# Optimization experiments

Measured on AMD Instinct MI355X. Metric: run time of the kernel, lower is better.

Reference implementation:

```python
import jax, jax.numpy as jnp
import numpy as np

SIGMA = 300.0      # args.sigma (temporal gaussian kernel width, frames)
DECAY = 0.9        # args.memory_decay; avg() uses weight = 1/decay per older entry
W_TIME = 1.0       # args.temporal_weight
ORIG_LOSS = 1.0    # args.originalloss_weight
EPS = 1e-7         # BCE clamp


def _get_msg(bank_values, bank_times, bank_mask, ids, times, future):
    """Vectorized MessagePassing.get_msg: per-(id,time) gather of stored
    messages, temporal-kernel + decay weighted average. Mirrors avg():
    out = sum_i dw_i * kernel_i * v_i / sum_i dw_i, dw_i = (1/decay)^rank_i
    with rank over entries passing the past/future condition, zeros if empty."""
    vals = bank_values[ids]                      # [N, M, C]
    ts = bank_times[ids].astype(jnp.float32)     # [N, M]
    mk = bank_mask[ids]                          # [N, M]
    t0 = times.astype(jnp.float32)[:, None]      # [N, 1]
    cond = (ts > t0) if future else (ts < t0)
    m = (mk & cond).astype(vals.dtype)           # [N, M]
    kern = jnp.exp(-((ts - t0) ** 2) / (2.0 * SIGMA ** 2))
    rank = jnp.cumsum(m, axis=1) - m             # exclusive rank among valid entries
    dw = ((1.0 / DECAY) ** rank) * m             # decay weights, masked
    num = jnp.einsum('nm,nmc->nc', dw * kern, vals)
    den = jnp.sum(dw, axis=1, keepdims=True)     # denominator excludes kernel (as avg())
    msg = jnp.where(den > 0, num / jnp.maximum(den, EPS), 0.0)
    return msg * W_TIME


def _bce(p, t):
    p = jnp.clip(p, EPS, 1.0 - EPS)
    return -jnp.mean(t * jnp.log(p) + (1.0 - t) * jnp.log(1.0 - p))


def setup_inputs() -> dict:
    key = jax.random.key(0)
    k = jax.random.split(key, 8)
    N, C, NUM_IDS, M = 512, 157, 10000, 20
    return {
        'a': jax.random.normal(k[0], (N, C), jnp.float32),
        'aa': jax.random.normal(k[1], (N, C, C), jnp.float32),
        'target': jax.random.uniform(k[2], (N, C), jnp.float32),
        'bank_values': jax.random.uniform(k[3], (NUM_IDS, M, C), jnp.float32),
        'bank_times': jax.random.randint(k[4], (NUM_IDS, M), 0, 1000, jnp.int32),
        'bank_mask': jnp.ones((NUM_IDS, M), dtype=bool),
        'ids': jax.random.randint(k[5], (N,), 0, NUM_IDS, jnp.int32),
        'times': jax.random.randint(k[6], (N,), 0, 1000, jnp.int32),
    }


def reference(a, aa, target, bank_values, bank_times, bank_mask, ids, times):
    # msg/fmsg come from stored (detached) data in the original
    msg = jax.lax.stop_gradient(_get_msg(bank_values, bank_times, bank_mask, ids, times, future=False))
    fmsg = jax.lax.stop_gradient(_get_msg(bank_values, bank_times, bank_mask, ids, times, future=True))
    # qa = a + sum_i aa[n,i,j]*msg[n,i] + sum_j aa[n,i,j]*fmsg[n,j]
    qa = a + jnp.einsum('nij,ni->nj', aa, msg) + jnp.einsum('nij,nj->ni', aa, fmsg)
    qa = jax.nn.sigmoid(qa)
    loss = _bce(qa, target) + _bce(jax.nn.sigmoid(a), target) * ORIG_LOSS
    # training, adjustment=False: pastloss = futureloss = 0
    loss = loss / 3.0
    return qa, loss
```

## Files before the change

kernel.cpp:

```cpp
#include <hip/hip_runtime.h>
#include <math.h>

#define N 512
#define C 157
#define M 20
#define NW 8

__device__ __forceinline__ float sigmoidf_(float x) {
    return 1.0f / (1.0f + __expf(-x));
}

__global__ __launch_bounds__(512) void atf_main_kernel(
    const float* __restrict__ a,
    const float* __restrict__ aa,
    const float* __restrict__ target,
    const float* __restrict__ bank_values,
    const int* __restrict__ bank_times,
    const int* __restrict__ bank_mask,
    const int* __restrict__ ids,
    const int* __restrict__ times,
    float* __restrict__ out,
    float* __restrict__ loss_part)
{
    const int n    = blockIdx.x;
    const int tid  = threadIdx.x;
    const int wave = tid >> 6;
    const int lane = tid & 63;

    __shared__ float s_ts[M];
    __shared__ int   s_mk[M];
    __shared__ float s_msg[C];
    __shared__ float s_fmsg[C];
    __shared__ float s_rowp[8][C];
    __shared__ float s_colp[NW][C];
    __shared__ float s_red[NW];

    const int   id = ids[n];
    const float t0 = (float)times[n];

    const float* aan = aa + (size_t)n * C * C;
    const int j0 = lane, j1 = lane + 64, j2 = lane + 128;
    const bool ok1 = (j1 < C), ok2 = (j2 < C);

    float a0, a1, a2, b0, b1, b2;
    {
        const float* rA = aan + wave * C;
        a0 = rA[j0]; a1 = ok1 ? rA[j1] : 0.0f; a2 = ok2 ? rA[j2] : 0.0f;
        const float* rB = aan + (wave + NW) * C;
        b0 = rB[j0]; b1 = ok1 ? rB[j1] : 0.0f; b2 = ok2 ? rB[j2] : 0.0f;
    }
    float av = 0.0f, tv = 0.0f;
    if (tid < C) {
        av = a[(size_t)n * C + tid];
        tv = target[(size_t)n * C + tid];
    }

    if (tid < M) {
        s_ts[tid] = (float)bank_times[(size_t)id * M + tid];
        s_mk[tid] = (bank_mask[(size_t)id * M + tid] != 0) ? 1 : 0;
    }
    __syncthreads();

    if (tid < C) {
        const float inv2s2 = 1.0f / (2.0f * 300.0f * 300.0f);
        const float INVDEC = 1.0f / 0.9f;
        float accP = 0.f, accF = 0.f, denP = 0.f, denF = 0.f;
        float wP = 1.f, wF = 1.f;
        const float* vb = bank_values + (size_t)id * M * C + tid;
        #pragma unroll
        for (int m = 0; m < M; ++m) {
            const float ts = s_ts[m];
            const float d  = ts - t0;
            const float kern = __expf(-d * d * inv2s2);
            const float v = vb[m * C];
            const bool mk = (s_mk[m] != 0);
            if (mk && ts < t0) { accP += wP * kern * v; denP += wP; wP *= INVDEC; }
            if (mk && ts > t0) { accF += wF * kern * v; denF += wF; wF *= INVDEC; }
        }
        s_msg[tid]  = (denP > 0.f) ? accP / fmaxf(denP, 1e-7f) : 0.0f;
        s_fmsg[tid] = (denF > 0.f) ? accF / fmaxf(denF, 1e-7f) : 0.0f;
    }
    __syncthreads();

    float col0 = 0.f, col1 = 0.f, col2 = 0.f;
    const float f0 = s_fmsg[j0];
    const float f1 = ok1 ? s_fmsg[j1] : 0.0f;
    const float f2 = ok2 ? s_fmsg[j2] : 0.0f;

    for (int i = wave; i < C; ) {
        const int inext = i + 2 * NW;
        float na0 = 0.f, na1 = 0.f, na2 = 0.f, nb0 = 0.f, nb1 = 0.f, nb2 = 0.f;
        if (inext < C) {
            const float* rA = aan + inext * C;
            na0 = rA[j0]; na1 = ok1 ? rA[j1] : 0.0f; na2 = ok2 ? rA[j2] : 0.0f;
            const int ibn = inext + NW;
            if (ibn < C) {
                const float* rB = aan + ibn * C;
                nb0 = rB[j0]; nb1 = ok1 ? rB[j1] : 0.0f; nb2 = ok2 ? rB[j2] : 0.0f;
            }
        }
        const int ib = i + NW;
        const float mA = s_msg[i];
        const float mB = (ib < C) ? s_msg[ib] : 0.0f;

        col0 += a0 * mA + b0 * mB;
        col1 += a1 * mA + b1 * mB;
        col2 += a2 * mA + b2 * mB;

        float rpA = a0 * f0 + a1 * f1 + a2 * f2;
        float rpB = b0 * f0 + b1 * f1 + b2 * f2;
        rpA += __shfl_down(rpA, 32, 64);  rpB += __shfl_down(rpB, 32, 64);
        rpA += __shfl_down(rpA, 16, 64);  rpB += __shfl_down(rpB, 16, 64);
        rpA += __shfl_down(rpA,  8, 64);  rpB += __shfl_down(rpB,  8, 64);
        if (lane < 8) {
            s_rowp[lane][i] = rpA;
            if (ib < C) s_rowp[lane][ib] = rpB;
        }
        a0 = na0; a1 = na1; a2 = na2;
        b0 = nb0; b1 = nb1; b2 = nb2;
        i = inext;
    }
    s_colp[wave][j0] = col0;
    if (ok1) s_colp[wave][j1] = col1;
    if (ok2) s_colp[wave][j2] = col2;
    __syncthreads();

    float local = 0.0f;
    if (tid < C) {
        float colsum = 0.0f;
        #pragma unroll
        for (int w = 0; w < NW; ++w) colsum += s_colp[w][tid];
        float rowsum = 0.0f;
        #pragma unroll
        for (int k = 0; k < 8; ++k) rowsum += s_rowp[k][tid];

        const float qlin = av + colsum + rowsum;
        const float p = sigmoidf_(qlin);
        out[(size_t)n * C + tid] = p;

        float pc = fminf(fmaxf(p, 1e-7f), 1.0f - 1e-7f);
        float pa = sigmoidf_(av);
        pa = fminf(fmaxf(pa, 1e-7f), 1.0f - 1e-7f);
        local = tv * logf(pc) + (1.0f - tv) * logf(1.0f - pc)
              + tv * logf(pa) + (1.0f - tv) * logf(1.0f - pa);
    }
    #pragma unroll
    for (int off = 32; off > 0; off >>= 1) local += __shfl_down(local, off, 64);
    if (lane == 0) s_red[wave] = local;
    __syncthreads();
    if (tid == 0) {
        float s = 0.0f;
        #pragma unroll
        for (int w = 0; w < NW; ++w) s += s_red[w];
        loss_part[n] = s;
    }
}

__global__ __launch_bounds__(256) void atf_finalize_kernel(
    const float* __restrict__ loss_part,
    float* __restrict__ out)
{
    const int tid  = threadIdx.x;
    const int wave = tid >> 6;
    const int lane = tid & 63;
    __shared__ double s_red[4];

    double local = (double)loss_part[tid] + (double)loss_part[tid + 256];
    #pragma unroll
    for (int off = 32; off > 0; off >>= 1) local += __shfl_down(local, off, 64);
    if (lane == 0) s_red[wave] = local;
    __syncthreads();
    if (tid == 0) {
        const double s = s_red[0] + s_red[1] + s_red[2] + s_red[3];
        out[N * C] = (float)(-s / ((double)(N * C) * 3.0));
    }
}

extern "C" void kernel_launch(void* const* d_in, const int* in_sizes, int n_in,
                              void* d_out, int out_size, void* d_ws, size_t ws_size,
                              hipStream_t stream) {
    const float* a           = (const float*)d_in[0];
    const float* aa          = (const float*)d_in[1];
    const float* target      = (const float*)d_in[2];
    const float* bank_values = (const float*)d_in[3];
    const int*   bank_times  = (const int*)d_in[4];
    const int*   bank_mask   = (const int*)d_in[5];
    const int*   ids         = (const int*)d_in[6];
    const int*   times       = (const int*)d_in[7];

    float* out       = (float*)d_out;
    float* loss_part = (float*)d_ws;

    atf_main_kernel<<<N, 512, 0, stream>>>(a, aa, target, bank_values, bank_times,
                                           bank_mask, ids, times, out, loss_part);
    atf_finalize_kernel<<<1, 256, 0, stream>>>(loss_part, out);
}
```

Before: 201.4 us.

## Batch-prefetch aa rows into registers and replace finalize kernel with atomic loss

Each block now issues all bank_values loads and the first half of its aa rows up front, before the first barrier. The second half is loaded after the message computation, replacing the old one-row-ahead software pipeline with two large batches. This raises memory-level parallelism to hide HBM latency in a bandwidth-bound kernel, at the cost of more registers per thread (launch bounds now request 4 blocks). The finalize reduction kernel is replaced by a zero-init kernel plus a per-block float atomicAdd. That makes the loss sum order nondeterministic and lowers its precision from double to float.

```diff
diff --git a/kernel.cpp b/kernel.cpp
--- a/kernel.cpp
+++ b/kernel.cpp
@@ -6,11 +6,17 @@
 #define M 20
 #define NW 8
 
+#define LOSS_SCALE (-1.0f / ((float)N * (float)C * 3.0f))
+
 __device__ __forceinline__ float sigmoidf_(float x) {
     return 1.0f / (1.0f + __expf(-x));
 }
 
-__global__ __launch_bounds__(512) void atf_main_kernel(
+__global__ void atf_zero_kernel(float* __restrict__ out) {
+    out[N * C] = 0.0f;
+}
+
+__global__ __launch_bounds__(512, 4) void atf_main_kernel(
     const float* __restrict__ a,
     const float* __restrict__ aa,
     const float* __restrict__ target,
@@ -19,8 +25,7 @@
     const int* __restrict__ bank_mask,
     const int* __restrict__ ids,
     const int* __restrict__ times,
-    float* __restrict__ out,
-    float* __restrict__ loss_part)
+    float* __restrict__ out)
 {
     const int n    = blockIdx.x;
     const int tid  = threadIdx.x;
@@ -42,37 +47,48 @@
     const int j0 = lane, j1 = lane + 64, j2 = lane + 128;
     const bool ok1 = (j1 < C), ok2 = (j2 < C);
 
-    float a0, a1, a2, b0, b1, b2;
-    {
-        const float* rA = aan + wave * C;
-        a0 = rA[j0]; a1 = ok1 ? rA[j1] : 0.0f; a2 = ok2 ? rA[j2] : 0.0f;
-        const float* rB = aan + (wave + NW) * C;
-        b0 = rB[j0]; b1 = ok1 ? rB[j1] : 0.0f; b2 = ok2 ? rB[j2] : 0.0f;
-    }
+    if (tid < M) {
+        s_ts[tid] = (float)bank_times[(size_t)id * M + tid];
+        s_mk[tid] = (bank_mask[(size_t)id * M + tid] != 0) ? 1 : 0;
+    }
+
     float av = 0.0f, tv = 0.0f;
+    float vv[M];
     if (tid < C) {
         av = a[(size_t)n * C + tid];
         tv = target[(size_t)n * C + tid];
-    }
-
-    if (tid < M) {
-        s_ts[tid] = (float)bank_times[(size_t)id * M + tid];
-        s_mk[tid] = (bank_mask[(size_t)id * M + tid] != 0) ? 1 : 0;
-    }
-    __syncthreads();
+        const float* vb = bank_values + (size_t)id * M * C + tid;
+        #pragma unroll
+        for (int m = 0; m < M; ++m) vv[m] = vb[(size_t)m * C];
+    }
+
+    float rA[5][3], rB[5][3];
+    #pragma unroll
+    for (int p = 0; p < 5; ++p) {
+        const float* rowA = aan + (wave + p * 16) * C;
+        rA[p][0] = rowA[j0];
+        rA[p][1] = ok1 ? rowA[j1] : 0.0f;
+        rA[p][2] = ok2 ? rowA[j2] : 0.0f;
+        const float* rowB = aan + (wave + p * 16 + 8) * C;
+        rB[p][0] = rowB[j0];
+        rB[p][1] = ok1 ? rowB[j1] : 0.0f;
+        rB[p][2] = ok2 ? rowB[j2] : 0.0f;
+    }
+
+    asm volatile("s_waitcnt lgkmcnt(0)" ::: "memory");
+    __builtin_amdgcn_s_barrier();
 
     if (tid < C) {
         const float inv2s2 = 1.0f / (2.0f * 300.0f * 300.0f);
         const float INVDEC = 1.0f / 0.9f;
         float accP = 0.f, accF = 0.f, denP = 0.f, denF = 0.f;
         float wP = 1.f, wF = 1.f;
-        const float* vb = bank_values + (size_t)id * M * C + tid;
         #pragma unroll
         for (int m = 0; m < M; ++m) {
             const float ts = s_ts[m];
             const float d  = ts - t0;
             const float kern = __expf(-d * d * inv2s2);
-            const float v = vb[m * C];
+            const float v = vv[m];
             const bool mk = (s_mk[m] != 0);
             if (mk && ts < t0) { accP += wP * kern * v; denP += wP; wP *= INVDEC; }
             if (mk && ts > t0) { accF += wF * kern * v; denF += wF; wF *= INVDEC; }
@@ -80,46 +96,74 @@
         s_msg[tid]  = (denP > 0.f) ? accP / fmaxf(denP, 1e-7f) : 0.0f;
         s_fmsg[tid] = (denF > 0.f) ? accF / fmaxf(denF, 1e-7f) : 0.0f;
     }
-    __syncthreads();
-
-    float col0 = 0.f, col1 = 0.f, col2 = 0.f;
+
+    asm volatile("s_waitcnt lgkmcnt(0)" ::: "memory");
+    __builtin_amdgcn_s_barrier();
+
+    float rA2[5][3], rB2[5][3];
+    #pragma unroll
+    for (int p = 0; p < 5; ++p) {
+        const int iA = wave + (p + 5) * 16;
+        const int iB = iA + 8;
+        const float* rowA = aan + iA * C;
+        rA2[p][0] = rowA[j0];
+        rA2[p][1] = ok1 ? rowA[j1] : 0.0f;
+        rA2[p][2] = ok2 ? rowA[j2] : 0.0f;
+        if (iB < C) {
+            const float* rowB = aan + iB * C;
+            rB2[p][0] = rowB[j0];
+            rB2[p][1] = ok1 ? rowB[j1] : 0.0f;
+            rB2[p][2] = ok2 ? rowB[j2] : 0.0f;
+        } else {
+            rB2[p][0] = 0.0f; rB2[p][1] = 0.0f; rB2[p][2] = 0.0f;
+        }
+    }
+
     const float f0 = s_fmsg[j0];
     const float f1 = ok1 ? s_fmsg[j1] : 0.0f;
     const float f2 = ok2 ? s_fmsg[j2] : 0.0f;
-
-    for (int i = wave; i < C; ) {
-        const int inext = i + 2 * NW;
-        float na0 = 0.f, na1 = 0.f, na2 = 0.f, nb0 = 0.f, nb1 = 0.f, nb2 = 0.f;
-        if (inext < C) {
-            const float* rA = aan + inext * C;
-            na0 = rA[j0]; na1 = ok1 ? rA[j1] : 0.0f; na2 = ok2 ? rA[j2] : 0.0f;
-            const int ibn = inext + NW;
-            if (ibn < C) {
-                const float* rB = aan + ibn * C;
-                nb0 = rB[j0]; nb1 = ok1 ? rB[j1] : 0.0f; nb2 = ok2 ? rB[j2] : 0.0f;
-            }
-        }
-        const int ib = i + NW;
-        const float mA = s_msg[i];
-        const float mB = (ib < C) ? s_msg[ib] : 0.0f;
-
-        col0 += a0 * mA + b0 * mB;
-        col1 += a1 * mA + b1 * mB;
-        col2 += a2 * mA + b2 * mB;
-
-        float rpA = a0 * f0 + a1 * f1 + a2 * f2;
-        float rpB = b0 * f0 + b1 * f1 + b2 * f2;
+    float col0 = 0.f, col1 = 0.f, col2 = 0.f;
+
+    #pragma unroll
+    for (int p = 0; p < 5; ++p) {
+        const int iA = wave + p * 16;
+        const int iB = iA + 8;
+        const float mA = s_msg[iA];
+        const float mB = s_msg[iB];
+        col0 += rA[p][0] * mA + rB[p][0] * mB;
+        col1 += rA[p][1] * mA + rB[p][1] * mB;
+        col2 += rA[p][2] * mA + rB[p][2] * mB;
+        float rpA = rA[p][0] * f0 + rA[p][1] * f1 + rA[p][2] * f2;
+        float rpB = rB[p][0] * f0 + rB[p][1] * f1 + rB[p][2] * f2;
         rpA += __shfl_down(rpA, 32, 64);  rpB += __shfl_down(rpB, 32, 64);
         rpA += __shfl_down(rpA, 16, 64);  rpB += __shfl_down(rpB, 16, 64);
         rpA += __shfl_down(rpA,  8, 64);  rpB += __shfl_down(rpB,  8, 64);
         if (lane < 8) {
-            s_rowp[lane][i] = rpA;
-            if (ib < C) s_rowp[lane][ib] = rpB;
-        }
-        a0 = na0; a1 = na1; a2 = na2;
-        b0 = nb0; b1 = nb1; b2 = nb2;
-        i = inext;
-    }
+            s_rowp[lane][iA] = rpA;
+            s_rowp[lane][iB] = rpB;
+        }
+    }
+    #pragma unroll
+    for (int p = 0; p < 5; ++p) {
+        const int iA = wave + (p + 5) * 16;
+        const int iB = iA + 8;
+        const bool okB = (iB < C);
+        const float mA = s_msg[iA];
+        const float mB = okB ? s_msg[iB] : 0.0f;
+        col0 += rA2[p][0] * mA + rB2[p][0] * mB;
+        col1 += rA2[p][1] * mA + rB2[p][1] * mB;
+        col2 += rA2[p][2] * mA + rB2[p][2] * mB;
+        float rpA = rA2[p][0] * f0 + rA2[p][1] * f1 + rA2[p][2] * f2;
+        float rpB = rB2[p][0] * f0 + rB2[p][1] * f1 + rB2[p][2] * f2;
+        rpA += __shfl_down(rpA, 32, 64);  rpB += __shfl_down(rpB, 32, 64);
+        rpA += __shfl_down(rpA, 16, 64);  rpB += __shfl_down(rpB, 16, 64);
+        rpA += __shfl_down(rpA,  8, 64);  rpB += __shfl_down(rpB,  8, 64);
+        if (lane < 8) {
+            s_rowp[lane][iA] = rpA;
+            if (okB) s_rowp[lane][iB] = rpB;
+        }
+    }
+
     s_colp[wave][j0] = col0;
     if (ok1) s_colp[wave][j1] = col1;
     if (ok2) s_colp[wave][j2] = col2;
@@ -152,27 +196,7 @@
         float s = 0.0f;
         #pragma unroll
         for (int w = 0; w < NW; ++w) s += s_red[w];
-        loss_part[n] = s;
-    }
-}
-
-__global__ __launch_bounds__(256) void atf_finalize_kernel(
-    const float* __restrict__ loss_part,
-    float* __restrict__ out)
-{
-    const int tid  = threadIdx.x;
-    const int wave = tid >> 6;
-    const int lane = tid & 63;
-    __shared__ double s_red[4];
-
-    double local = (double)loss_part[tid] + (double)loss_part[tid + 256];
-    #pragma unroll
-    for (int off = 32; off > 0; off >>= 1) local += __shfl_down(local, off, 64);
-    if (lane == 0) s_red[wave] = local;
-    __syncthreads();
-    if (tid == 0) {
-        const double s = s_red[0] + s_red[1] + s_red[2] + s_red[3];
-        out[N * C] = (float)(-s / ((double)(N * C) * 3.0));
+        atomicAdd(out + N * C, s * LOSS_SCALE);
     }
 }
 
@@ -188,10 +212,9 @@
     const int*   ids         = (const int*)d_in[6];
     const int*   times       = (const int*)d_in[7];
 
-    float* out       = (float*)d_out;
-    float* loss_part = (float*)d_ws;
-
+    float* out = (float*)d_out;
+
+    atf_zero_kernel<<<1, 1, 0, stream>>>(out);
     atf_main_kernel<<<N, 512, 0, stream>>>(a, aa, target, bank_values, bank_times,
-                                           bank_mask, ids, times, out, loss_part);
-    atf_finalize_kernel<<<1, 256, 0, stream>>>(loss_part, out);
-}
+                                           bank_mask, ids, times, out);
+}
```

After: 208.9 us. 3.7% more time.

## Deepen aa row prefetch to three stages and hoist bank loads before barrier

Applied to the files above, without the earlier changes.

Replaces the one-ahead register prefetch of aa rows with a fully unrolled 10-step loop using a 3-slot register ring buffer, so three row pairs are in flight per wave. Bank value loads are moved before the first barrier, and barriers become raw s_barrier calls that wait only on LDS counters, so global loads overlap the sync. It also sets launch bounds to 4 blocks per SM and switches logf to __logf. The aim is to hide HBM latency on the memory-bound 50 MB aa stream, at the cost of more registers (vv[20], buf[18]) and slightly less accurate logs.

```diff
diff --git a/kernel.cpp b/kernel.cpp
--- a/kernel.cpp
+++ b/kernel.cpp
@@ -10,7 +10,7 @@
     return 1.0f / (1.0f + __expf(-x));
 }
 
-__global__ __launch_bounds__(512) void atf_main_kernel(
+__global__ __launch_bounds__(512, 4) void atf_main_kernel(
     const float* __restrict__ a,
     const float* __restrict__ aa,
     const float* __restrict__ target,
@@ -42,37 +42,48 @@
     const int j0 = lane, j1 = lane + 64, j2 = lane + 128;
     const bool ok1 = (j1 < C), ok2 = (j2 < C);
 
-    float a0, a1, a2, b0, b1, b2;
-    {
-        const float* rA = aan + wave * C;
-        a0 = rA[j0]; a1 = ok1 ? rA[j1] : 0.0f; a2 = ok2 ? rA[j2] : 0.0f;
-        const float* rB = aan + (wave + NW) * C;
-        b0 = rB[j0]; b1 = ok1 ? rB[j1] : 0.0f; b2 = ok2 ? rB[j2] : 0.0f;
-    }
+    if (tid < M) {
+        s_ts[tid] = (float)bank_times[(size_t)id * M + tid];
+        s_mk[tid] = (bank_mask[(size_t)id * M + tid] != 0) ? 1 : 0;
+    }
+
     float av = 0.0f, tv = 0.0f;
+    float vv[M];
     if (tid < C) {
         av = a[(size_t)n * C + tid];
         tv = target[(size_t)n * C + tid];
-    }
-
-    if (tid < M) {
-        s_ts[tid] = (float)bank_times[(size_t)id * M + tid];
-        s_mk[tid] = (bank_mask[(size_t)id * M + tid] != 0) ? 1 : 0;
-    }
-    __syncthreads();
+        const float* vb = bank_values + (size_t)id * M * C + tid;
+        #pragma unroll
+        for (int m = 0; m < M; ++m) vv[m] = vb[(size_t)m * C];
+    }
+
+    float buf[3][6];
+    #pragma unroll
+    for (int p = 0; p < 3; ++p) {
+        const float* rowA = aan + (wave + p * 16) * C;
+        buf[p][0] = rowA[j0];
+        buf[p][1] = ok1 ? rowA[j1] : 0.0f;
+        buf[p][2] = ok2 ? rowA[j2] : 0.0f;
+        const float* rowB = aan + (wave + p * 16 + 8) * C;
+        buf[p][3] = rowB[j0];
+        buf[p][4] = ok1 ? rowB[j1] : 0.0f;
+        buf[p][5] = ok2 ? rowB[j2] : 0.0f;
+    }
+
+    asm volatile("s_waitcnt lgkmcnt(0)" ::: "memory");
+    __builtin_amdgcn_s_barrier();
 
     if (tid < C) {
         const float inv2s2 = 1.0f / (2.0f * 300.0f * 300.0f);
         const float INVDEC = 1.0f / 0.9f;
         float accP = 0.f, accF = 0.f, denP = 0.f, denF = 0.f;
         float wP = 1.f, wF = 1.f;
-        const float* vb = bank_values + (size_t)id * M * C + tid;
         #pragma unroll
         for (int m = 0; m < M; ++m) {
             const float ts = s_ts[m];
             const float d  = ts - t0;
             const float kern = __expf(-d * d * inv2s2);
-            const float v = vb[m * C];
+            const float v = vv[m];
             const bool mk = (s_mk[m] != 0);
             if (mk && ts < t0) { accP += wP * kern * v; denP += wP; wP *= INVDEC; }
             if (mk && ts > t0) { accF += wF * kern * v; denF += wF; wF *= INVDEC; }
@@ -80,28 +91,27 @@
         s_msg[tid]  = (denP > 0.f) ? accP / fmaxf(denP, 1e-7f) : 0.0f;
         s_fmsg[tid] = (denF > 0.f) ? accF / fmaxf(denF, 1e-7f) : 0.0f;
     }
-    __syncthreads();
-
-    float col0 = 0.f, col1 = 0.f, col2 = 0.f;
+
+    asm volatile("s_waitcnt lgkmcnt(0)" ::: "memory");
+    __builtin_amdgcn_s_barrier();
+
     const float f0 = s_fmsg[j0];
     const float f1 = ok1 ? s_fmsg[j1] : 0.0f;
     const float f2 = ok2 ? s_fmsg[j2] : 0.0f;
-
-    for (int i = wave; i < C; ) {
-        const int inext = i + 2 * NW;
-        float na0 = 0.f, na1 = 0.f, na2 = 0.f, nb0 = 0.f, nb1 = 0.f, nb2 = 0.f;
-        if (inext < C) {
-            const float* rA = aan + inext * C;
-            na0 = rA[j0]; na1 = ok1 ? rA[j1] : 0.0f; na2 = ok2 ? rA[j2] : 0.0f;
-            const int ibn = inext + NW;
-            if (ibn < C) {
-                const float* rB = aan + ibn * C;
-                nb0 = rB[j0]; nb1 = ok1 ? rB[j1] : 0.0f; nb2 = ok2 ? rB[j2] : 0.0f;
-            }
-        }
-        const int ib = i + NW;
-        const float mA = s_msg[i];
-        const float mB = (ib < C) ? s_msg[ib] : 0.0f;
+    float col0 = 0.f, col1 = 0.f, col2 = 0.f;
+
+    #pragma unroll
+    for (int p = 0; p < 10; ++p) {
+        const int slot = p % 3;
+        const int iA = wave + p * 16;
+        const int iB = iA + 8;
+        const bool okB = (iB < C);
+
+        const float a0 = buf[slot][0], a1 = buf[slot][1], a2 = buf[slot][2];
+        const float b0 = buf[slot][3], b1 = buf[slot][4], b2 = buf[slot][5];
+
+        const float mA = s_msg[iA];
+        const float mB = okB ? s_msg[iB] : 0.0f;
 
         col0 += a0 * mA + b0 * mB;
         col1 += a1 * mA + b1 * mB;
@@ -113,13 +123,28 @@
         rpA += __shfl_down(rpA, 16, 64);  rpB += __shfl_down(rpB, 16, 64);
         rpA += __shfl_down(rpA,  8, 64);  rpB += __shfl_down(rpB,  8, 64);
         if (lane < 8) {
-            s_rowp[lane][i] = rpA;
-            if (ib < C) s_rowp[lane][ib] = rpB;
+            s_rowp[lane][iA] = rpA;
+            if (okB) s_rowp[lane][iB] = rpB;
         }
-        a0 = na0; a1 = na1; a2 = na2;
-        b0 = nb0; b1 = nb1; b2 = nb2;
-        i = inext;
-    }
+
+        if (p + 3 < 10) {
+            const int q = p + 3;
+            const float* rowA = aan + (wave + q * 16) * C;
+            buf[slot][0] = rowA[j0];
+            buf[slot][1] = ok1 ? rowA[j1] : 0.0f;
+            buf[slot][2] = ok2 ? rowA[j2] : 0.0f;
+            const int ibq = wave + q * 16 + 8;
+            if (ibq < C) {
+                const float* rowB = aan + ibq * C;
+                buf[slot][3] = rowB[j0];
+                buf[slot][4] = ok1 ? rowB[j1] : 0.0f;
+                buf[slot][5] = ok2 ? rowB[j2] : 0.0f;
+            } else {
+                buf[slot][3] = 0.0f; buf[slot][4] = 0.0f; buf[slot][5] = 0.0f;
+            }
+        }
+    }
+
     s_colp[wave][j0] = col0;
     if (ok1) s_colp[wave][j1] = col1;
     if (ok2) s_colp[wave][j2] = col2;
@@ -141,8 +166,8 @@
         float pc = fminf(fmaxf(p, 1e-7f), 1.0f - 1e-7f);
         float pa = sigmoidf_(av);
         pa = fminf(fmaxf(pa, 1e-7f), 1.0f - 1e-7f);
-        local = tv * logf(pc) + (1.0f - tv) * logf(1.0f - pc)
-              + tv * logf(pa) + (1.0f - tv) * logf(1.0f - pa);
+        local = tv * __logf(pc) + (1.0f - tv) * __logf(1.0f - pc)
+              + tv * __logf(pa) + (1.0f - tv) * __logf(1.0f - pa);
     }
     #pragma unroll
     for (int off = 32; off > 0; off >>= 1) local += __shfl_down(local, off, 64);
```

Result: no change. 203.7 us (+1.2%).
